# Performance work log

Measured on AMD Instinct MI355X. Metric: run time of the kernel, lower is better.

Reference implementation:

```python
import jax, jax.numpy as jnp
import numpy as np

B, S, H = 8, 8192, 512

def setup_inputs() -> dict:
    key = jax.random.key(0)
    k1, k2, k3, k4 = jax.random.split(key, 4)
    hidden = jax.random.normal(k1, (1, B, H), dtype=jnp.float32)
    encoder_outputs = jax.random.normal(k2, (B, S, H), dtype=jnp.float32)
    W = jax.random.normal(k3, (H, H), dtype=jnp.float32) * (1.0 / np.sqrt(H))
    b = jax.random.normal(k4, (H,), dtype=jnp.float32) * 0.01
    return {"hidden": hidden, "encoder_outputs": encoder_outputs, "W": W, "b": b}

def reference(hidden, encoder_outputs, W, b):
    # method='general': energy_k = Linear(enc[:,k]) ; score_k = bmm(energy_k[:,None,:], hidden.permute(1,2,0)).sum()
    # hidden: [1,B,H] -> h: [B,H]
    h = hidden[0]
    proj = jnp.einsum('bsh,kh->bsk', encoder_outputs, W) + b  # Linear: x @ W.T + b -> [B,S,H]
    attn_energies = jnp.einsum('bsh,bh->bs', proj, h)         # [B,S]
    return jax.nn.softmax(attn_energies, axis=1)
```

## Files before the change

kernel.cpp:

```cpp
#include <hip/hip_runtime.h>
#include <math.h>

#define Hd 512
#define Bn 8
#define Sn 8192
#define KC 16

__global__ __launch_bounds__(256) void k_proj(const float* __restrict__ hidden,
                                              const float* __restrict__ W,
                                              float* __restrict__ vpart) {
    const int b  = blockIdx.x;
    const int kc = blockIdx.y;
    const int t  = threadIdx.x;
    __shared__ float hs[32];
    if (t < 32) hs[t] = hidden[b * Hd + kc * 32 + t];
    __syncthreads();
    float acc0 = 0.f, acc1 = 0.f;
    const float* Wp = W + (size_t)(kc * 32) * Hd;
    #pragma unroll
    for (int k = 0; k < 32; ++k) {
        const float hk = hs[k];
        acc0 += hk * Wp[(size_t)k * Hd + t];
        acc1 += hk * Wp[(size_t)k * Hd + t + 256];
    }
    float* vo = vpart + ((size_t)kc * Bn + b) * Hd;
    vo[t]       = acc0;
    vo[t + 256] = acc1;
}

__global__ __launch_bounds__(256) void k_energy(const float* __restrict__ enc,
                                                const float* __restrict__ vpart,
                                                float* __restrict__ e) {
    const int b    = blockIdx.y;
    const int wave = threadIdx.x >> 6;
    const int lane = threadIdx.x & 63;

    float4 v0 = make_float4(0.f, 0.f, 0.f, 0.f);
    float4 v1 = make_float4(0.f, 0.f, 0.f, 0.f);
    #pragma unroll 4
    for (int kc = 0; kc < KC; ++kc) {
        const float4* sp = (const float4*)(vpart + ((size_t)kc * Bn + b) * Hd);
        const float4 a = sp[lane];
        const float4 c = sp[64 + lane];
        v0.x += a.x; v0.y += a.y; v0.z += a.z; v0.w += a.w;
        v1.x += c.x; v1.y += c.y; v1.z += c.z; v1.w += c.w;
    }

    const int row0 = blockIdx.x * 32 + wave * 8;
    const float4* base = (const float4*)(enc + ((size_t)b * Sn + row0) * Hd);

    #pragma unroll
    for (int rb = 0; rb < 8; rb += 4) {
        float p[4];
        #pragma unroll
        for (int r = 0; r < 4; ++r) {
            const float4* rowp = base + (size_t)(rb + r) * (Hd / 4);
            const float4 a0 = rowp[lane];
            const float4 a1 = rowp[64 + lane];
            p[r] = a0.x * v0.x + a0.y * v0.y + a0.z * v0.z + a0.w * v0.w
                 + a1.x * v1.x + a1.y * v1.y + a1.z * v1.z + a1.w * v1.w;
        }
        float s0 = p[0] + __shfl_xor(p[0], 1, 64);
        float s1 = p[1] + __shfl_xor(p[1], 1, 64);
        float s2 = p[2] + __shfl_xor(p[2], 1, 64);
        float s3 = p[3] + __shfl_xor(p[3], 1, 64);
        float t0 = (lane & 1) ? s1 : s0;
        float t1 = (lane & 1) ? s3 : s2;
        t0 += __shfl_xor(t0, 2, 64);
        t1 += __shfl_xor(t1, 2, 64);
        float w = (lane & 2) ? t1 : t0;
        w += __shfl_xor(w, 4, 64);
        w += __shfl_xor(w, 8, 64);
        w += __shfl_xor(w, 16, 64);
        w += __shfl_xor(w, 32, 64);
        if (lane < 4) e[(size_t)b * Sn + row0 + rb + lane] = w;
    }
}

__global__ __launch_bounds__(1024) void k_softmax(const float* __restrict__ e,
                                                  float* __restrict__ out) {
    const int b = blockIdx.x;
    const int t = threadIdx.x;
    const int wave = t >> 6, lane = t & 63;
    const float* eb = e + (size_t)b * Sn;

    float vals[8];
    float m = -INFINITY;
    #pragma unroll
    for (int i = 0; i < 8; ++i) {
        vals[i] = eb[t + i * 1024];
        m = fmaxf(m, vals[i]);
    }
    #pragma unroll
    for (int off = 32; off >= 1; off >>= 1)
        m = fmaxf(m, __shfl_xor(m, off, 64));

    __shared__ float red[16];
    if (lane == 0) red[wave] = m;
    __syncthreads();
    if (t < 16) {
        float mm = red[t];
        #pragma unroll
        for (int off = 8; off >= 1; off >>= 1)
            mm = fmaxf(mm, __shfl_xor(mm, off, 16));
        if (t == 0) red[0] = mm;
    }
    __syncthreads();
    m = red[0];
    __syncthreads();

    float s = 0.f;
    #pragma unroll
    for (int i = 0; i < 8; ++i) {
        vals[i] = __expf(vals[i] - m);
        s += vals[i];
    }
    #pragma unroll
    for (int off = 32; off >= 1; off >>= 1)
        s += __shfl_xor(s, off, 64);
    if (lane == 0) red[wave] = s;
    __syncthreads();
    if (t < 16) {
        float ss = red[t];
        #pragma unroll
        for (int off = 8; off >= 1; off >>= 1)
            ss += __shfl_xor(ss, off, 16);
        if (t == 0) red[0] = ss;
    }
    __syncthreads();
    const float inv = 1.0f / red[0];

    #pragma unroll
    for (int i = 0; i < 8; ++i)
        out[(size_t)b * Sn + t + i * 1024] = vals[i] * inv;
}

extern "C" void kernel_launch(void* const* d_in, const int* in_sizes, int n_in,
                              void* d_out, int out_size, void* d_ws, size_t ws_size,
                              hipStream_t stream) {
    const float* hidden = (const float*)d_in[0];
    const float* enc    = (const float*)d_in[1];
    const float* W      = (const float*)d_in[2];
    float* out = (float*)d_out;

    float* vpart = (float*)d_ws;
    float* e     = vpart + KC * Bn * Hd;

    k_proj   <<<dim3(Bn, KC),      256,  0, stream>>>(hidden, W, vpart);
    k_energy <<<dim3(Sn / 32, Bn), 256,  0, stream>>>(enc, vpart, e);
    k_softmax<<<Bn,                1024, 0, stream>>>(e, out);
}
```

Before: 35.38 us.

## Fuse per-block softmax partials into energy kernel and parallelize finalize

The energy kernel now computes a local max and sum-of-exp for each 32-row block and writes them as partials. A new finalize kernel merges these partials with an online-softmax reduction and normalizes across 128 blocks, replacing the old softmax that ran only 8 blocks. The projection kernel now computes the full v vector in 8 blocks instead of 16 K-chunk partials, so the energy kernel no longer sums chunks. The projection loses parallelism (8 blocks reading all of W serially), which could lengthen that stage.

```diff
diff --git a/kernel.cpp b/kernel.cpp
--- a/kernel.cpp
+++ b/kernel.cpp
@@ -4,49 +4,41 @@
 #define Hd 512
 #define Bn 8
 #define Sn 8192
-#define KC 16
+#define SB 256
 
-__global__ __launch_bounds__(256) void k_proj(const float* __restrict__ hidden,
+__global__ __launch_bounds__(512) void k_proj(const float* __restrict__ hidden,
                                               const float* __restrict__ W,
-                                              float* __restrict__ vpart) {
-    const int b  = blockIdx.x;
-    const int kc = blockIdx.y;
-    const int t  = threadIdx.x;
-    __shared__ float hs[32];
-    if (t < 32) hs[t] = hidden[b * Hd + kc * 32 + t];
-    __syncthreads();
-    float acc0 = 0.f, acc1 = 0.f;
-    const float* Wp = W + (size_t)(kc * 32) * Hd;
-    #pragma unroll
-    for (int k = 0; k < 32; ++k) {
-        const float hk = hs[k];
-        acc0 += hk * Wp[(size_t)k * Hd + t];
-        acc1 += hk * Wp[(size_t)k * Hd + t + 256];
+                                              float* __restrict__ v) {
+    const int b = blockIdx.x;
+    const int h = threadIdx.x;
+    float a0 = 0.f, a1 = 0.f, a2 = 0.f, a3 = 0.f;
+    #pragma unroll 4
+    for (int k = 0; k < Hd; k += 4) {
+        const float4 hv = *(const float4*)(hidden + b * Hd + k);
+        a0 += hv.x * W[(size_t)(k + 0) * Hd + h];
+        a1 += hv.y * W[(size_t)(k + 1) * Hd + h];
+        a2 += hv.z * W[(size_t)(k + 2) * Hd + h];
+        a3 += hv.w * W[(size_t)(k + 3) * Hd + h];
     }
-    float* vo = vpart + ((size_t)kc * Bn + b) * Hd;
-    vo[t]       = acc0;
-    vo[t + 256] = acc1;
+    v[b * Hd + h] = (a0 + a1) + (a2 + a3);
 }
 
 __global__ __launch_bounds__(256) void k_energy(const float* __restrict__ enc,
-                                                const float* __restrict__ vpart,
-                                                float* __restrict__ e) {
+                                                const float* __restrict__ v,
+                                                float* __restrict__ e,
+                                                float2* __restrict__ partials) {
+    const int sb   = blockIdx.x;
     const int b    = blockIdx.y;
-    const int wave = threadIdx.x >> 6;
-    const int lane = threadIdx.x & 63;
+    const int t    = threadIdx.x;
+    const int wave = t >> 6, lane = t & 63;
 
-    float4 v0 = make_float4(0.f, 0.f, 0.f, 0.f);
-    float4 v1 = make_float4(0.f, 0.f, 0.f, 0.f);
-    #pragma unroll 4
-    for (int kc = 0; kc < KC; ++kc) {
-        const float4* sp = (const float4*)(vpart + ((size_t)kc * Bn + b) * Hd);
-        const float4 a = sp[lane];
-        const float4 c = sp[64 + lane];
-        v0.x += a.x; v0.y += a.y; v0.z += a.z; v0.w += a.w;
-        v1.x += c.x; v1.y += c.y; v1.z += c.z; v1.w += c.w;
-    }
+    __shared__ float sm[32];
 
-    const int row0 = blockIdx.x * 32 + wave * 8;
+    const float4* vp = (const float4*)(v + b * Hd);
+    const float4 v0 = vp[lane];
+    const float4 v1 = vp[64 + lane];
+
+    const int row0 = sb * 32 + wave * 8;
     const float4* base = (const float4*)(enc + ((size_t)b * Sn + row0) * Hd);
 
     #pragma unroll
@@ -73,66 +65,54 @@
         w += __shfl_xor(w, 8, 64);
         w += __shfl_xor(w, 16, 64);
         w += __shfl_xor(w, 32, 64);
-        if (lane < 4) e[(size_t)b * Sn + row0 + rb + lane] = w;
+        if (lane < 4) sm[wave * 8 + rb + lane] = w;
+    }
+    __syncthreads();
+
+    if (wave == 0) {
+        const float ev = (lane < 32) ? sm[lane] : -INFINITY;
+        float m = ev;
+        #pragma unroll
+        for (int off = 32; off >= 1; off >>= 1)
+            m = fmaxf(m, __shfl_xor(m, off, 64));
+        float l = (lane < 32) ? __expf(ev - m) : 0.f;
+        #pragma unroll
+        for (int off = 32; off >= 1; off >>= 1)
+            l += __shfl_xor(l, off, 64);
+        if (lane < 32) e[(size_t)b * Sn + sb * 32 + lane] = ev;
+        if (lane == 0) partials[b * SB + sb] = make_float2(m, l);
     }
 }
 
-__global__ __launch_bounds__(1024) void k_softmax(const float* __restrict__ e,
+__global__ __launch_bounds__(512) void k_finalize(const float* __restrict__ e,
+                                                  const float2* __restrict__ partials,
                                                   float* __restrict__ out) {
-    const int b = blockIdx.x;
-    const int t = threadIdx.x;
-    const int wave = t >> 6, lane = t & 63;
-    const float* eb = e + (size_t)b * Sn;
+    const int b    = blockIdx.y;
+    const int t    = threadIdx.x;
+    const int lane = t & 63;
 
-    float vals[8];
-    float m = -INFINITY;
+    const float2* pp = partials + b * SB;
+    float2 p0 = pp[lane];
+    float M = p0.x, L = p0.y;
     #pragma unroll
-    for (int i = 0; i < 8; ++i) {
-        vals[i] = eb[t + i * 1024];
-        m = fmaxf(m, vals[i]);
+    for (int i = 1; i < 4; ++i) {
+        const float2 pi = pp[lane + 64 * i];
+        const float Mn = fmaxf(M, pi.x);
+        L = L * __expf(M - Mn) + pi.y * __expf(pi.x - Mn);
+        M = Mn;
     }
     #pragma unroll
-    for (int off = 32; off >= 1; off >>= 1)
-        m = fmaxf(m, __shfl_xor(m, off, 64));
+    for (int off = 32; off >= 1; off >>= 1) {
+        const float Mo = __shfl_xor(M, off, 64);
+        const float Lo = __shfl_xor(L, off, 64);
+        const float Mn = fmaxf(M, Mo);
+        L = L * __expf(M - Mn) + Lo * __expf(Mo - Mn);
+        M = Mn;
+    }
+    const float inv = 1.0f / L;
 
-    __shared__ float red[16];
-    if (lane == 0) red[wave] = m;
-    __syncthreads();
-    if (t < 16) {
-        float mm = red[t];
-        #pragma unroll
-        for (int off = 8; off >= 1; off >>= 1)
-            mm = fmaxf(mm, __shfl_xor(mm, off, 16));
-        if (t == 0) red[0] = mm;
-    }
-    __syncthreads();
-    m = red[0];
-    __syncthreads();
-
-    float s = 0.f;
-    #pragma unroll
-    for (int i = 0; i < 8; ++i) {
-        vals[i] = __expf(vals[i] - m);
-        s += vals[i];
-    }
-    #pragma unroll
-    for (int off = 32; off >= 1; off >>= 1)
-        s += __shfl_xor(s, off, 64);
-    if (lane == 0) red[wave] = s;
-    __syncthreads();
-    if (t < 16) {
-        float ss = red[t];
-        #pragma unroll
-        for (int off = 8; off >= 1; off >>= 1)
-            ss += __shfl_xor(ss, off, 16);
-        if (t == 0) red[0] = ss;
-    }
-    __syncthreads();
-    const float inv = 1.0f / red[0];
-
-    #pragma unroll
-    for (int i = 0; i < 8; ++i)
-        out[(size_t)b * Sn + t + i * 1024] = vals[i] * inv;
+    const size_t j = (size_t)b * Sn + blockIdx.x * 512 + t;
+    out[j] = __expf(e[j] - M) * inv;
 }
 
 extern "C" void kernel_launch(void* const* d_in, const int* in_sizes, int n_in,
@@ -143,10 +123,11 @@
     const float* W      = (const float*)d_in[2];
     float* out = (float*)d_out;
 
-    float* vpart = (float*)d_ws;
-    float* e     = vpart + KC * Bn * Hd;
+    float*  v        = (float*)d_ws;
+    float2* partials = (float2*)(v + Bn * Hd);
+    float*  e        = (float*)(partials + Bn * SB);
 
-    k_proj   <<<dim3(Bn, KC),      256,  0, stream>>>(hidden, W, vpart);
-    k_energy <<<dim3(Sn / 32, Bn), 256,  0, stream>>>(enc, vpart, e);
-    k_softmax<<<Bn,                1024, 0, stream>>>(e, out);
+    k_proj    <<<Bn,              512, 0, stream>>>(hidden, W, v);
+    k_energy  <<<dim3(SB, Bn),    256, 0, stream>>>(enc, v, e, partials);
+    k_finalize<<<dim3(16, Bn),    512, 0, stream>>>(e, partials, out);
 }
```

New measurement: 43.10 us. +21.8%, slower.
